# Optimization experiments

Hardware: AMD Instinct MI355X
Metric: run time of the kernel (lower is better)

The kernel has to match this reference:

```python
import jax, jax.numpy as jnp
import numpy as np
import math

B, S, D, H = 2, 1024, 4096, 32
HD = D // H          # head_dim = 128
P = 10               # prompt_len
THETA = 500000.0     # rope_theta


def _rope(t, cos, sin):
    # t: [b, s, h, hd]; pairs (2i, 2i+1) form complex numbers as in view_as_complex
    tr = t[..., 0::2]
    ti = t[..., 1::2]
    c = cos[None, :, None, :]
    s = sin[None, :, None, :]
    out = jnp.stack([tr * c - ti * s, tr * s + ti * c], axis=-1)  # [b,s,h,hd/2,2]
    return out.reshape(t.shape)


def setup_inputs() -> dict:
    key = jax.random.key(0)
    ks = jax.random.split(key, 8)
    sc = 0.02
    x = jax.random.normal(ks[0], (B, S, D), jnp.float32)
    wq = jax.random.normal(ks[1], (D, D), jnp.float32) * sc
    wk = jax.random.normal(ks[2], (D, D), jnp.float32) * sc
    wv = jax.random.normal(ks[3], (D, D), jnp.float32) * sc
    wo = jax.random.normal(ks[4], (D, D), jnp.float32) * sc
    prompt = jax.random.normal(ks[5], (P, D), jnp.float32)
    prompt_gate = jax.random.normal(ks[6], (1, H, 1, 1), jnp.float32) * 0.1
    # RoPE tables (real/imag of freqs_cis)
    inv = 1.0 / (THETA ** (jnp.arange(0, HD, 2, dtype=jnp.float32) / HD))  # [HD/2]
    ang = jnp.outer(jnp.arange(S, dtype=jnp.float32), inv)                 # [S, HD/2]
    freqs_cos = jnp.cos(ang)
    freqs_sin = jnp.sin(ang)
    # causal additive mask
    mask = jnp.triu(jnp.full((S, S), -1e9, jnp.float32), 1)[None, None]
    type_weight = jax.random.uniform(ks[7], (B, S, 1), jnp.float32)
    return dict(x=x, wq=wq, wk=wk, wv=wv, wo=wo, prompt=prompt,
                prompt_gate=prompt_gate, freqs_cos=freqs_cos,
                freqs_sin=freqs_sin, mask=mask, type_weight=type_weight,
                start_pos=0)


def reference(x, wq, wk, wv, wo, prompt, prompt_gate, freqs_cos, freqs_sin,
              mask, type_weight, start_pos):
    # training-mode forward: start_pos == 0, keys/values = current tokens
    scale = 1.0 / math.sqrt(HD)
    xq = (x @ wq.T).reshape(B, S, H, HD)
    xk = (x @ wk.T).reshape(B, S, H, HD)
    xv = (x @ wv.T).reshape(B, S, H, HD)
    xq = _rope(xq, freqs_cos, freqs_sin)
    xk = _rope(xk, freqs_cos, freqs_sin)
    q = xq.transpose(0, 2, 1, 3)  # [b,h,s,hd]
    k = xk.transpose(0, 2, 1, 3)
    v = xv.transpose(0, 2, 1, 3)
    scores = jnp.einsum('bhqd,bhkd->bhqk', q, k) * scale + mask
    probs = jax.nn.softmax(scores, axis=-1)
    out = jnp.einsum('bhqk,bhkd->bhqd', probs, v)  # [b,h,s,hd]
    # gated prompt injection (num_experts == 1); type_weight unused, as in source
    pk = (prompt @ wk.T).reshape(P, H, HD)
    pv = (prompt @ wv.T).reshape(P, H, HD)
    p_scores = jnp.einsum('bhqd,phd->bhqp', q, pk) * scale
    p_probs = prompt_gate * jax.nn.softmax(p_scores, axis=-1)
    p_out = jnp.einsum('bhqp,phd->bhqd', p_probs, pv)
    out = (out + p_out).transpose(0, 2, 1, 3).reshape(B, S, D)
    return out @ wo.T
```

## Files before the change

### kernel.cpp

```cpp
#include <hip/hip_runtime.h>
#include <hip/hip_bf16.h>
#include <stdint.h>

typedef __hip_bfloat16 bf16;
typedef __attribute__((ext_vector_type(8))) short short8;
typedef __attribute__((ext_vector_type(4))) float f32x4;

#define SCALE_ 0.08838834764831845f

static __device__ __forceinline__ float bf2f(short u) {
  unsigned int x = ((unsigned int)(unsigned short)u) << 16;
  return __builtin_bit_cast(float, x);
}
static __device__ __forceinline__ short f2bf(float f) {
  __hip_bfloat16 h = __float2bfloat16(f);
  return __builtin_bit_cast(short, h);
}
static __device__ __forceinline__ f32x4 mfma16(short8 a, short8 b, f32x4 c) {
  return __builtin_amdgcn_mfma_f32_16x16x32_bf16(a, b, c, 0, 0, 0);
}
static __device__ __forceinline__ void gl_lds16(const bf16* g, bf16* l) {
  __builtin_amdgcn_global_load_lds(
      (const __attribute__((address_space(1))) unsigned int*)g,
      (__attribute__((address_space(3))) unsigned int*)l, 16, 0, 0);
}

__global__ __launch_bounds__(256) void cvt6(
    const float* __restrict__ sx, const float* __restrict__ sq,
    const float* __restrict__ sk, const float* __restrict__ sv,
    const float* __restrict__ so, const float* __restrict__ sp,
    bf16* __restrict__ dx, bf16* __restrict__ dq, bf16* __restrict__ dk,
    bf16* __restrict__ dv, bf16* __restrict__ d4, bf16* __restrict__ dp)
{
  int b = blockIdx.x;
  const float* s; bf16* d; int off;
  if (b < 4096)       { s = sx; d = dx; off = b; }
  else if (b < 12288) { s = sq; d = dq; off = b - 4096; }
  else if (b < 20480) { s = sk; d = dk; off = b - 12288; }
  else if (b < 28672) { s = sv; d = dv; off = b - 20480; }
  else if (b < 36864) { s = so; d = d4; off = b - 28672; }
  else                { s = sp; d = dp; off = b - 36864; }
  long base = (long)off * 2048 + threadIdx.x * 8;
  f32x4 a = *(const f32x4*)(s + base);
  f32x4 c = *(const f32x4*)(s + base + 4);
  short8 o;
#pragma unroll
  for (int j = 0; j < 4; j++) { o[j] = f2bf(a[j]); o[4 + j] = f2bf(c[j]); }
  *(short8*)(d + base) = o;
}

template <int NKT, bool KSPLIT>
__global__ __launch_bounds__(512, 2) void gemm_bt(
    const bf16* __restrict__ A, const bf16* __restrict__ A2,
    const bf16* __restrict__ B0, const bf16* __restrict__ B1, const bf16* __restrict__ B2w,
    bf16* __restrict__ C0, bf16* __restrict__ C1, bf16* __restrict__ C2,
    bf16* __restrict__ P1, bf16* __restrict__ P2,
    float* __restrict__ CF,
    int M1, int Mtot)
{
  __shared__ char lds[131072];
  const int tid = threadIdx.x, w = tid >> 6, l = tid & 63;
  const int lr = l & 15, lg = l >> 4;
  const int wm = w >> 2, wn = w & 3;
  const int z = blockIdx.z;
  const bf16* Bw = KSPLIT ? B0 : ((z == 0) ? B0 : ((z == 1) ? B1 : B2w));
  bf16* C  = (z == 0) ? C0 : ((z == 1) ? C1 : C2);
  bf16* Cp = (KSPLIT || z == 0) ? (bf16*)0 : ((z == 1) ? P1 : P2);
  float* CFz = CF;
  long koff = 0;
  if (KSPLIT) { koff = (long)z * NKT * 64; CFz = CF + (long)z * M1 * 4096; }

  const int cpx = gridDim.x >> 3, orig = blockIdx.x;
  const int wg = (orig & 7) * cpx + (orig >> 3);
  const long m0 = (long)(wg >> 4) * 256;
  const long n0 = (long)(wg & 15) * 256;

  const int r0 = ((tid >> 3) << 1) | ((tid >> 2) & 1);
  const int c0 = (tid & 3) ^ ((tid >> 3) & 3);
  const bf16 *pa0, *pa1;
  {
    long mx = (long)(Mtot - M1) - 1;
    long g0 = m0 + r0, g1 = m0 + r0 + 128;
    const bf16 *q0, *q1;
    if (g0 < M1) q0 = A + g0 * 4096;
    else { long rr = g0 - M1; if (rr > mx) rr = mx; q0 = A2 + rr * 4096; }
    if (g1 < M1) q1 = A + g1 * 4096;
    else { long rr = g1 - M1; if (rr > mx) rr = mx; q1 = A2 + rr * 4096; }
    pa0 = q0 + c0 * 8 + koff;
    pa1 = q1 + c0 * 8 + koff;
  }
  const bf16* pb0 = Bw + (n0 + r0) * 4096 + c0 * 8 + koff;
  const bf16* pb1 = pb0 + (long)128 * 4096;

  const int ro  = (lr >> 1) * 128 + (((lr & 1) * 4) + (lg ^ ((lr >> 1) & 3))) * 16;
  const int aro = wm * 8192 + ro;
  const int bro = wn * 4096 + ro;

  f32x4 acc[8][4];
#pragma unroll
  for (int i = 0; i < 8; i++)
#pragma unroll
    for (int j = 0; j < 4; j++) acc[i][j] = (f32x4){0.f, 0.f, 0.f, 0.f};

  short8 af[4], bf[4];

#define STGA(S_, KE_)                                                        \
  {                                                                          \
    bf16* d_ = (bf16*)(lds + (S_) * 16384) + tid * 8;                        \
    gl_lds16(pa0 + (KE_), d_);                                               \
    gl_lds16(pa1 + (KE_), d_ + 4096);                                        \
  }
#define STGB(S_, KE_)                                                        \
  {                                                                          \
    bf16* d_ = (bf16*)(lds + (S_) * 16384) + tid * 8;                        \
    gl_lds16(pb0 + (KE_), d_);                                               \
    gl_lds16(pb1 + (KE_), d_ + 4096);                                        \
  }
#define SYNC(VM_)                                                            \
  {                                                                          \
    asm volatile("s_waitcnt vmcnt(" VM_ ")" ::: "memory");                   \
    __builtin_amdgcn_s_barrier();                                            \
    __builtin_amdgcn_sched_barrier(0);                                       \
  }
#define PHASE(PRB_, AU_, BU_, MO_, LB_, STG_)                                \
  {                                                                          \
    STG_                                                                     \
    const char* ab_ = lds + (PRB_) + (AU_) + aro;                            \
    _Pragma("unroll") for (int mi = 0; mi < 4; mi++)                         \
      af[mi] = *(const short8*)(ab_ + ((MO_) + mi) * 1024);                  \
    if (LB_) {                                                               \
      const char* bb_ = lds + (PRB_) + (BU_) + bro;                          \
      _Pragma("unroll") for (int ni = 0; ni < 4; ni++)                       \
        bf[ni] = *(const short8*)(bb_ + ni * 1024);                          \
    }                                                                        \
    asm volatile("s_waitcnt lgkmcnt(0)" ::: "memory");                       \
    __builtin_amdgcn_sched_barrier(0);                                       \
    __builtin_amdgcn_s_setprio(1);                                           \
    _Pragma("unroll") for (int mi = 0; mi < 4; mi++)                         \
      _Pragma("unroll") for (int ni = 0; ni < 4; ni++)                       \
        acc[(MO_) + mi][ni] = mfma16(af[mi], bf[ni], acc[(MO_) + mi][ni]);   \
    __builtin_amdgcn_s_setprio(0);                                           \
  }
#define KT(PRB_, S6_, S7_, S8_, S9_, KE1_, KE2_)                             \
  SYNC("8") PHASE(PRB_, 0, 16384, 0, 1, STGA(S6_, KE1_))                     \
  PHASE(PRB_, 0, 16384, 4, 0, STGB(S7_, KE1_))                               \
  SYNC("8") PHASE(PRB_, 32768, 49152, 0, 1, STGA(S8_, KE2_))                 \
  PHASE(PRB_, 32768, 49152, 4, 0, STGB(S9_, KE2_))

  STGA(0, 0) STGB(1, 0) STGA(2, 32) STGB(3, 32) STGA(4, 64) STGB(5, 64)

  for (int t = 0; t < NKT - 2; t += 2) {
    const int ka = (t + 1) * 64 + 32, kb = (t + 2) * 64;
    const int kc = (t + 2) * 64 + 32, kd = (t + 3) * 64;
    KT(0, 6, 7, 0, 1, ka, kb)
    KT(65536, 2, 3, 4, 5, kc, kd)
  }
  {
    const int kel = (NKT - 1) * 64 + 32;
    SYNC("8") PHASE(0, 0, 16384, 0, 1, STGA(6, kel))
    PHASE(0, 0, 16384, 4, 0, STGB(7, kel))
    SYNC("8") PHASE(0, 32768, 49152, 0, 1, )
    PHASE(0, 32768, 49152, 4, 0, )
  }
  SYNC("4") PHASE(65536, 0, 16384, 0, 1, )
  PHASE(65536, 0, 16384, 4, 0, )
  SYNC("0") PHASE(65536, 32768, 49152, 0, 1, )
  PHASE(65536, 32768, 49152, 4, 0, )

#undef KT
#undef PHASE
#undef SYNC
#undef STGB
#undef STGA

#pragma unroll
  for (int mi = 0; mi < 8; mi++) {
#pragma unroll
    for (int ni = 0; ni < 4; ni++) {
      long col = n0 + wn * 64 + ni * 16 + lr;
      f32x4 v = acc[mi][ni];
#pragma unroll
      for (int j = 0; j < 4; j++) {
        long row = m0 + wm * 128 + mi * 16 + lg * 4 + j;
        if (CFz) {
          CFz[row * 4096 + col] = v[j];
        } else if (row < M1) {
          *(short*)(C + row * 4096 + col) = f2bf(v[j]);
        } else if (Cp != 0 && row < Mtot) {
          *(short*)(Cp + (row - M1) * 4096 + col) = f2bf(v[j]);
        }
      }
    }
  }
}

__global__ __launch_bounds__(256) void addf(
    const float* __restrict__ p0, const float* __restrict__ p1,
    float* __restrict__ out)
{
  long i = ((long)blockIdx.x * 256 + threadIdx.x) * 4;
  f32x4 a = *(const f32x4*)(p0 + i);
  f32x4 b = *(const f32x4*)(p1 + i);
#pragma unroll
  for (int j = 0; j < 4; j++) a[j] += b[j];
  *(f32x4*)(out + i) = a;
}

__global__ __launch_bounds__(256) void rope_qk(
    bf16* __restrict__ Q, bf16* __restrict__ Kb,
    const float* __restrict__ FC, const float* __restrict__ FS)
{
  const int row = blockIdx.x;
  const int s = row & 1023;
  const int t = threadIdx.x;
  bf16* base = (blockIdx.y ? Kb : Q) + (long)row * 4096 + t * 16;
  short8 v0 = *(const short8*)base;
  short8 v1 = *(const short8*)(base + 8);
  const float* cp = FC + s * 64 + (t & 7) * 8;
  const float* sp = FS + s * 64 + (t & 7) * 8;
  f32x4 c0 = *(const f32x4*)cp;
  f32x4 c1 = *(const f32x4*)(cp + 4);
  f32x4 s0 = *(const f32x4*)sp;
  f32x4 s1 = *(const f32x4*)(sp + 4);
  short8 o0, o1;
#pragma unroll
  for (int j = 0; j < 4; j++) {
    float c = c0[j], sn = s0[j];
    float e = bf2f(v0[2 * j]), od = bf2f(v0[2 * j + 1]);
    o0[2 * j] = f2bf(e * c - od * sn);
    o0[2 * j + 1] = f2bf(e * sn + od * c);
    float c2 = c1[j], sn2 = s1[j];
    float e2 = bf2f(v1[2 * j]), od2 = bf2f(v1[2 * j + 1]);
    o1[2 * j] = f2bf(e2 * c2 - od2 * sn2);
    o1[2 * j + 1] = f2bf(e2 * sn2 + od2 * c2);
  }
  *(short8*)base = o0;
  *(short8*)(base + 8) = o1;
}

__global__ __launch_bounds__(256) void transpose_v(
    const bf16* __restrict__ V, bf16* __restrict__ VT)
{
  __shared__ bf16 T[64 * 128];
  const int tid = threadIdx.x;
  const int st = blockIdx.x * 64, bh = blockIdx.y;
  const int b = bh >> 5, h = bh & 31;
  const bf16* src = V + ((long)(b * 1024 + st)) * 4096 + h * 128;
#pragma unroll
  for (int rr = 0; rr < 4; ++rr) {
    int i = tid + rr * 256;
    int s_l = i >> 4, c = i & 15;
    short8 v = *(const short8*)(src + (long)s_l * 4096 + c * 8);
    *(short8*)((char*)T + s_l * 256 + ((c ^ (s_l & 7)) * 16)) = v;
  }
  __syncthreads();
#pragma unroll
  for (int rr = 0; rr < 4; ++rr) {
    int i = tid + rr * 256;
    int d = i >> 3, cs = i & 7;
    short8 ov;
#pragma unroll
    for (int e = 0; e < 8; e++) {
      int s_l = cs * 8 + e;
      ov[e] = *(const short*)((char*)T + s_l * 256 + (((d >> 3) ^ (s_l & 7)) * 16) + (d & 7) * 2);
    }
    *(short8*)(VT + ((long)bh * 128 + d) * 1024 + st + cs * 8) = ov;
  }
}

__global__ __launch_bounds__(256) void flash_attn(
    const bf16* __restrict__ Q, const bf16* __restrict__ Kg, const bf16* __restrict__ VT,
    const bf16* __restrict__ PK, const bf16* __restrict__ PV,
    const float* __restrict__ GATE, bf16* __restrict__ O)
{
  __shared__ bf16 Kl[32 * 128];
  __shared__ bf16 Vl[128 * 32];
  __shared__ bf16 PKl[16 * 128];
  __shared__ bf16 PVl[128 * 16];
  __shared__ bf16 Pl[4][16 * 32];
  const int tid = threadIdx.x, w = tid >> 6, l = tid & 63;
  const int lg = l >> 4, lr = l & 15;
  const int qb = blockIdx.x, bh = blockIdx.y;
  const int b = bh >> 5, h = bh & 31;
  const int q0 = qb * 64 + w * 16;

  short8 qf[4];
  {
    const bf16* qp = Q + ((long)(b * 1024 + q0 + lr)) * 4096 + h * 128 + lg * 8;
#pragma unroll
    for (int c = 0; c < 4; c++) qf[c] = *(const short8*)(qp + c * 32);
  }
  {
    int rowp = tid >> 4, pc = tid & 15, lc = pc ^ (rowp & 7);
    short8 v = {0, 0, 0, 0, 0, 0, 0, 0};
    if (rowp < 10) v = *(const short8*)(PK + (long)rowp * 4096 + h * 128 + lc * 8);
    *(short8*)((char*)PKl + tid * 16) = v;
  }
  {
    int d = tid >> 1, pb = (tid & 1) * 8;
#pragma unroll
    for (int e = 0; e < 8; e++) {
      int p = pb + e;
      short v = 0;
      if (p < 10) v = __builtin_bit_cast(short, PV[(long)p * 4096 + h * 128 + d]);
      *(short*)((char*)PVl + d * 32 + (((p >> 3) ^ (d & 1)) * 16) + (p & 7) * 2) = v;
    }
  }
  const float gate = GATE[h];

  f32x4 o[8];
#pragma unroll
  for (int i = 0; i < 8; i++) o[i] = (f32x4){0.f, 0.f, 0.f, 0.f};
  float m_[4] = {-1e30f, -1e30f, -1e30f, -1e30f};
  float l_[4] = {0.f, 0.f, 0.f, 0.f};

  const int nt = (qb + 1) * 2;
  const bf16* Kbase = Kg + ((long)b * 1024) * 4096 + h * 128;
  const bf16* Vbase = VT + ((long)bh) * 128 * 1024;
  const int cb1 = w * 64, cb2 = 256 + w * 64;
  const int iA = cb1 + l, iB = cb2 + l;
  bf16* pw = &Pl[w][0];

  for (int j = 0; j < nt; ++j) {
    __syncthreads();
    {
      const bf16* gA = Kbase + (long)(j * 32 + (iA >> 4)) * 4096 + ((iA & 15) ^ ((iA >> 4) & 7)) * 8;
      const bf16* gB = Kbase + (long)(j * 32 + (iB >> 4)) * 4096 + ((iB & 15) ^ ((iB >> 4) & 7)) * 8;
      gl_lds16(gA, Kl + cb1 * 8);
      gl_lds16(gB, Kl + cb2 * 8);
      const bf16* vA = Vbase + (long)(iA >> 2) * 1024 + j * 32 + ((iA & 3) ^ ((iA >> 2) & 3)) * 8;
      const bf16* vB = Vbase + (long)(iB >> 2) * 1024 + j * 32 + ((iB & 3) ^ ((iB >> 2) & 3)) * 8;
      gl_lds16(vA, Vl + cb1 * 8);
      gl_lds16(vB, Vl + cb2 * 8);
    }
    __syncthreads();

    f32x4 s[2];
#pragma unroll
    for (int ns = 0; ns < 2; ns++) {
      f32x4 a = (f32x4){0.f, 0.f, 0.f, 0.f};
      int krow = ns * 16 + lr;
      const char* kp = (const char*)Kl + krow * 256;
      int sw = krow & 7;
#pragma unroll
      for (int c = 0; c < 4; c++) {
        short8 kf = *(const short8*)(kp + (((c * 4 + lg) ^ sw) * 16));
        a = mfma16(qf[c], kf, a);
      }
      int key = j * 32 + krow;
#pragma unroll
      for (int r = 0; r < 4; r++) {
        int qr = q0 + lg * 4 + r;
        s[ns][r] = a[r] * SCALE_ + ((key <= qr) ? 0.0f : -1e30f);
      }
    }
    float mx[4], cor[4], sum[4];
#pragma unroll
    for (int r = 0; r < 4; r++) mx[r] = fmaxf(s[0][r], s[1][r]);
#pragma unroll
    for (int xm = 1; xm < 16; xm <<= 1)
#pragma unroll
      for (int r = 0; r < 4; r++) mx[r] = fmaxf(mx[r], __shfl_xor(mx[r], xm, 64));
#pragma unroll
    for (int r = 0; r < 4; r++) {
      float mn = fmaxf(m_[r], mx[r]);
      cor[r] = __expf(m_[r] - mn);
      m_[r] = mn;
      s[0][r] = __expf(s[0][r] - mn);
      s[1][r] = __expf(s[1][r] - mn);
      sum[r] = s[0][r] + s[1][r];
    }
#pragma unroll
    for (int xm = 1; xm < 16; xm <<= 1)
#pragma unroll
      for (int r = 0; r < 4; r++) sum[r] += __shfl_xor(sum[r], xm, 64);
#pragma unroll
    for (int r = 0; r < 4; r++) l_[r] = l_[r] * cor[r] + sum[r];
#pragma unroll
    for (int df = 0; df < 8; df++)
#pragma unroll
      for (int r = 0; r < 4; r++) o[df][r] *= cor[r];

#pragma unroll
    for (int ns = 0; ns < 2; ns++)
#pragma unroll
      for (int r = 0; r < 4; r++)
        *(short*)((char*)pw + ((lg * 4 + r) * 32 + ns * 16 + lr) * 2) = f2bf(s[ns][r]);
    asm volatile("s_waitcnt lgkmcnt(0)" ::: "memory");
    __builtin_amdgcn_sched_barrier(0);
    short8 pf = *(const short8*)(pw + lr * 32 + lg * 8);

#pragma unroll
    for (int df = 0; df < 8; df++) {
      int d = df * 16 + lr;
      short8 vf = *(const short8*)((const char*)Vl + d * 64 + ((lg ^ (d & 3)) * 16));
      o[df] = mfma16(pf, vf, o[df]);
    }
  }

  f32x4 ps;
  {
    f32x4 a = (f32x4){0.f, 0.f, 0.f, 0.f};
    const char* kp = (const char*)PKl + lr * 256;
    int sw = lr & 7;
#pragma unroll
    for (int c = 0; c < 4; c++) {
      short8 kf = *(const short8*)(kp + (((c * 4 + lg) ^ sw) * 16));
      a = mfma16(qf[c], kf, a);
    }
#pragma unroll
    for (int r = 0; r < 4; r++) ps[r] = (lr < 10) ? a[r] * SCALE_ : -1e30f;
  }
  {
    float pm[4], pss[4];
#pragma unroll
    for (int r = 0; r < 4; r++) pm[r] = ps[r];
#pragma unroll
    for (int xm = 1; xm < 16; xm <<= 1)
#pragma unroll
      for (int r = 0; r < 4; r++) pm[r] = fmaxf(pm[r], __shfl_xor(pm[r], xm, 64));
#pragma unroll
    for (int r = 0; r < 4; r++) { ps[r] = __expf(ps[r] - pm[r]); pss[r] = ps[r]; }
#pragma unroll
    for (int xm = 1; xm < 16; xm <<= 1)
#pragma unroll
      for (int r = 0; r < 4; r++) pss[r] += __shfl_xor(pss[r], xm, 64);
#pragma unroll
    for (int r = 0; r < 4; r++) ps[r] = ps[r] / pss[r];
  }
#pragma unroll
  for (int r = 0; r < 4; r++) {
    *(short*)((char*)pw + ((lg * 4 + r) * 32 + lr) * 2) = f2bf(ps[r]);
    *(short*)((char*)pw + ((lg * 4 + r) * 32 + 16 + lr) * 2) = 0;
  }
  asm volatile("s_waitcnt lgkmcnt(0)" ::: "memory");
  __builtin_amdgcn_sched_barrier(0);
  short8 pf2 = *(const short8*)(pw + lr * 32 + lg * 8);
  f32x4 po[8];
#pragma unroll
  for (int df = 0; df < 8; df++) {
    int d = df * 16 + lr;
    short8 vf = {0, 0, 0, 0, 0, 0, 0, 0};
    if (lg < 2) vf = *(const short8*)((const char*)PVl + d * 32 + ((lg ^ (d & 1)) * 16));
    po[df] = mfma16(pf2, vf, (f32x4){0.f, 0.f, 0.f, 0.f});
  }

  bf16* op = O + ((long)(b * 1024 + q0 + lg * 4)) * 4096 + h * 128 + lr;
#pragma unroll
  for (int df = 0; df < 8; df++)
#pragma unroll
    for (int r = 0; r < 4; r++) {
      float val = o[df][r] / l_[r] + gate * po[df][r];
      *(short*)(op + (long)r * 4096 + df * 16) = f2bf(val);
    }
}

extern "C" void kernel_launch(void* const* d_in, const int* in_sizes, int n_in,
                              void* d_out, int out_size, void* d_ws, size_t ws_size,
                              hipStream_t stream) {
  (void)in_sizes; (void)n_in; (void)out_size; (void)ws_size;
  const float* x      = (const float*)d_in[0];
  const float* wq     = (const float*)d_in[1];
  const float* wk     = (const float*)d_in[2];
  const float* wv     = (const float*)d_in[3];
  const float* wo     = (const float*)d_in[4];
  const float* prompt = (const float*)d_in[5];
  const float* gate   = (const float*)d_in[6];
  const float* fcos   = (const float*)d_in[7];
  const float* fsin   = (const float*)d_in[8];
  float* out = (float*)d_out;
  char* ws = (char*)d_ws;

  size_t o = 0;
  bf16* xb  = (bf16*)(ws + o); o += (size_t)8388608 * 2;
  bf16* wqb = (bf16*)(ws + o); o += (size_t)16777216 * 2;
  bf16* wkb = (bf16*)(ws + o); o += (size_t)16777216 * 2;
  bf16* wvb = (bf16*)(ws + o); o += (size_t)16777216 * 2;
  bf16* wob = (bf16*)(ws + o); o += (size_t)16777216 * 2;
  bf16* pb  = (bf16*)(ws + o); o += (size_t)40960 * 2;
  bf16* q_ws  = (bf16*)(ws + o); o += (size_t)2048 * 4096 * 2;
  bf16* k_ws  = (bf16*)(ws + o); o += (size_t)2048 * 4096 * 2;
  bf16* v_ws  = (bf16*)(ws + o); o += (size_t)2048 * 4096 * 2;
  bf16* vT_ws = (bf16*)(ws + o); o += (size_t)2048 * 4096 * 2;
  bf16* pk_ws = (bf16*)(ws + o); o += (size_t)40960 * 2;
  bf16* pv_ws = (bf16*)(ws + o); o += (size_t)40960 * 2;
  bf16* attn_ws = v_ws;
  float* p0 = (float*)q_ws;
  float* p1 = (float*)xb;

  cvt6<<<dim3(36884), 256, 0, stream>>>(x, wq, wk, wv, wo, prompt,
                                        xb, wqb, wkb, wvb, wob, pb);
  gemm_bt<64, false><<<dim3(144, 1, 3), 512, 0, stream>>>(
      xb, pb, wqb, wkb, wvb, q_ws, k_ws, v_ws, pk_ws, pv_ws, (float*)0, 2048, 2058);
  rope_qk<<<dim3(2048, 2), 256, 0, stream>>>(q_ws, k_ws, fcos, fsin);
  transpose_v<<<dim3(16, 64), 256, 0, stream>>>(v_ws, vT_ws);
  flash_attn<<<dim3(16, 64), 256, 0, stream>>>(
      q_ws, k_ws, vT_ws, pk_ws, pv_ws, gate, attn_ws);
  gemm_bt<32, true><<<dim3(128, 1, 2), 512, 0, stream>>>(
      attn_ws, attn_ws, wob, wob, wob, (bf16*)0, (bf16*)0, (bf16*)0,
      (bf16*)0, (bf16*)0, p0, 2048, 2048);
  addf<<<dim3(8192), 256, 0, stream>>>(p0, p0 + (size_t)2048 * 4096, out);
}
```

Before: 524.9 us.

## Replace split-K output GEMM with 256x128-tile kernel, fuse rope and V transpose

The output projection previously ran as a split-K GEMM writing two fp32 partials, followed by a separate add kernel. It now uses a dedicated 256x128-tile GEMM with a three-stage global-to-LDS pipeline and an XCD-aware block remap, writing fp32 output directly over the full K. This removes the partial-sum traffic and the extra launch, at the cost of fewer blocks (256) and a longer K loop per block. RoPE and the V transpose are also merged into one launch to save a kernel launch.

```diff
diff --git a/kernel.cpp b/kernel.cpp
--- a/kernel.cpp
+++ b/kernel.cpp
@@ -194,61 +194,154 @@
   }
 }
 
-__global__ __launch_bounds__(256) void addf(
-    const float* __restrict__ p0, const float* __restrict__ p1,
-    float* __restrict__ out)
+__global__ __launch_bounds__(512, 2) void gemm_n128(
+    const bf16* __restrict__ A, const bf16* __restrict__ Bw,
+    float* __restrict__ CF)
 {
-  long i = ((long)blockIdx.x * 256 + threadIdx.x) * 4;
-  f32x4 a = *(const f32x4*)(p0 + i);
-  f32x4 b = *(const f32x4*)(p1 + i);
-#pragma unroll
-  for (int j = 0; j < 4; j++) a[j] += b[j];
-  *(f32x4*)(out + i) = a;
-}
-
-__global__ __launch_bounds__(256) void rope_qk(
+  __shared__ char lds[98304];
+  const int tid = threadIdx.x, w = tid >> 6, l = tid & 63;
+  const int lr = l & 15, lg = l >> 4;
+  const int wm = w >> 1, wn = w & 1;
+
+  const int cpx = gridDim.x >> 3, orig = blockIdx.x;
+  const int wg = (orig & 7) * cpx + (orig >> 3);
+  const long m0 = (long)(wg >> 5) * 256;
+  const long n0 = (long)(wg & 31) * 128;
+
+  const int r0 = ((tid >> 3) << 1) | ((tid >> 2) & 1);
+  const int c0 = (tid & 3) ^ ((tid >> 3) & 3);
+  const bf16* pa0 = A + (m0 + r0) * 4096 + c0 * 8;
+  const bf16* pa1 = pa0 + (long)128 * 4096;
+  const bf16* pb0 = Bw + (n0 + r0) * 4096 + c0 * 8;
+
+  const int ro  = (lr >> 1) * 128 + (((lr & 1) * 4) + (lg ^ ((lr >> 1) & 3))) * 16;
+  const int aro = wm * 4096 + ro;
+  const int bro = wn * 4096 + ro;
+
+  f32x4 acc[4][4];
+#pragma unroll
+  for (int i = 0; i < 4; i++)
+#pragma unroll
+    for (int j = 0; j < 4; j++) acc[i][j] = (f32x4){0.f, 0.f, 0.f, 0.f};
+
+  short8 af[4], bf[4];
+
+#define NSTGA(SB_, KE_)                                                      \
+  {                                                                          \
+    bf16* d_ = (bf16*)(lds + (SB_)) + tid * 8;                               \
+    gl_lds16(pa0 + (KE_), d_);                                               \
+    gl_lds16(pa1 + (KE_), d_ + 4096);                                        \
+  }
+#define NSTGB(SB_, KE_)                                                      \
+  {                                                                          \
+    bf16* d_ = (bf16*)(lds + (SB_)) + tid * 8;                               \
+    gl_lds16(pb0 + (KE_), d_);                                               \
+  }
+#define NSYNC(VM_)                                                           \
+  {                                                                          \
+    asm volatile("s_waitcnt vmcnt(" VM_ ")" ::: "memory");                   \
+    __builtin_amdgcn_s_barrier();                                            \
+    __builtin_amdgcn_sched_barrier(0);                                       \
+  }
+#define NPH(PRB_, AO_, BO_, STG_)                                            \
+  {                                                                          \
+    STG_                                                                     \
+    const char* ab_ = lds + (PRB_) + (AO_) + aro;                            \
+    _Pragma("unroll") for (int mi = 0; mi < 4; mi++)                         \
+      af[mi] = *(const short8*)(ab_ + mi * 1024);                            \
+    const char* bb_ = lds + (PRB_) + (BO_) + bro;                            \
+    _Pragma("unroll") for (int ni = 0; ni < 4; ni++)                         \
+      bf[ni] = *(const short8*)(bb_ + ni * 1024);                            \
+    asm volatile("s_waitcnt lgkmcnt(0)" ::: "memory");                       \
+    __builtin_amdgcn_sched_barrier(0);                                       \
+    __builtin_amdgcn_s_setprio(1);                                           \
+    _Pragma("unroll") for (int mi = 0; mi < 4; mi++)                         \
+      _Pragma("unroll") for (int ni = 0; ni < 4; ni++)                       \
+        acc[mi][ni] = mfma16(af[mi], bf[ni], acc[mi][ni]);                   \
+    __builtin_amdgcn_s_setprio(0);                                           \
+  }
+
+  NSTGA(0, 0)      NSTGB(16384, 0)
+  NSTGA(24576, 32) NSTGB(40960, 32)
+  NSTGA(49152, 64) NSTGB(65536, 64)
+
+  for (int t = 0; t < 62; t += 2) {
+    const int ka = (t + 1) * 64 + 32;
+    const int kb = (t + 2) * 64;
+    NSYNC("3") NPH(0, 0, 16384,     NSTGA(49152 + 24576, ka) NSTGB(49152 + 40960, ka))
+    NSYNC("3") NPH(0, 24576, 40960, NSTGA(0, kb) NSTGB(16384, kb))
+    const int kc = (t + 2) * 64 + 32;
+    const int kd = (t + 3) * 64;
+    NSYNC("3") NPH(49152, 0, 16384,     NSTGA(24576, kc) NSTGB(40960, kc))
+    NSYNC("3") NPH(49152, 24576, 40960, NSTGA(49152, kd) NSTGB(49152 + 16384, kd))
+  }
+  NSYNC("3") NPH(0, 0, 16384,     NSTGA(49152 + 24576, 63 * 64 + 32) NSTGB(49152 + 40960, 63 * 64 + 32))
+  NSYNC("3") NPH(0, 24576, 40960, )
+  NSYNC("3") NPH(49152, 0, 16384, )
+  NSYNC("0") NPH(49152, 24576, 40960, )
+
+#undef NPH
+#undef NSYNC
+#undef NSTGB
+#undef NSTGA
+
+#pragma unroll
+  for (int mi = 0; mi < 4; mi++) {
+#pragma unroll
+    for (int ni = 0; ni < 4; ni++) {
+      long col = n0 + wn * 64 + ni * 16 + lr;
+      f32x4 v = acc[mi][ni];
+#pragma unroll
+      for (int j = 0; j < 4; j++) {
+        long row = m0 + wm * 64 + mi * 16 + lg * 4 + j;
+        CF[row * 4096 + col] = v[j];
+      }
+    }
+  }
+}
+
+__global__ __launch_bounds__(256) void prep_qkv(
     bf16* __restrict__ Q, bf16* __restrict__ Kb,
-    const float* __restrict__ FC, const float* __restrict__ FS)
-{
-  const int row = blockIdx.x;
-  const int s = row & 1023;
-  const int t = threadIdx.x;
-  bf16* base = (blockIdx.y ? Kb : Q) + (long)row * 4096 + t * 16;
-  short8 v0 = *(const short8*)base;
-  short8 v1 = *(const short8*)(base + 8);
-  const float* cp = FC + s * 64 + (t & 7) * 8;
-  const float* sp = FS + s * 64 + (t & 7) * 8;
-  f32x4 c0 = *(const f32x4*)cp;
-  f32x4 c1 = *(const f32x4*)(cp + 4);
-  f32x4 s0 = *(const f32x4*)sp;
-  f32x4 s1 = *(const f32x4*)(sp + 4);
-  short8 o0, o1;
-#pragma unroll
-  for (int j = 0; j < 4; j++) {
-    float c = c0[j], sn = s0[j];
-    float e = bf2f(v0[2 * j]), od = bf2f(v0[2 * j + 1]);
-    o0[2 * j] = f2bf(e * c - od * sn);
-    o0[2 * j + 1] = f2bf(e * sn + od * c);
-    float c2 = c1[j], sn2 = s1[j];
-    float e2 = bf2f(v1[2 * j]), od2 = bf2f(v1[2 * j + 1]);
-    o1[2 * j] = f2bf(e2 * c2 - od2 * sn2);
-    o1[2 * j + 1] = f2bf(e2 * sn2 + od2 * c2);
-  }
-  *(short8*)base = o0;
-  *(short8*)(base + 8) = o1;
-}
-
-__global__ __launch_bounds__(256) void transpose_v(
+    const float* __restrict__ FC, const float* __restrict__ FS,
     const bf16* __restrict__ V, bf16* __restrict__ VT)
 {
+  const int t = threadIdx.x;
+  if (blockIdx.y < 2) {
+    const int row = blockIdx.x;
+    const int s = row & 1023;
+    bf16* base = (blockIdx.y ? Kb : Q) + (long)row * 4096 + t * 16;
+    short8 v0 = *(const short8*)base;
+    short8 v1 = *(const short8*)(base + 8);
+    const float* cp = FC + s * 64 + (t & 7) * 8;
+    const float* sp = FS + s * 64 + (t & 7) * 8;
+    f32x4 c0 = *(const f32x4*)cp;
+    f32x4 c1 = *(const f32x4*)(cp + 4);
+    f32x4 s0 = *(const f32x4*)sp;
+    f32x4 s1 = *(const f32x4*)(sp + 4);
+    short8 o0, o1;
+#pragma unroll
+    for (int j = 0; j < 4; j++) {
+      float c = c0[j], sn = s0[j];
+      float e = bf2f(v0[2 * j]), od = bf2f(v0[2 * j + 1]);
+      o0[2 * j] = f2bf(e * c - od * sn);
+      o0[2 * j + 1] = f2bf(e * sn + od * c);
+      float c2 = c1[j], sn2 = s1[j];
+      float e2 = bf2f(v1[2 * j]), od2 = bf2f(v1[2 * j + 1]);
+      o1[2 * j] = f2bf(e2 * c2 - od2 * sn2);
+      o1[2 * j + 1] = f2bf(e2 * sn2 + od2 * c2);
+    }
+    *(short8*)base = o0;
+    *(short8*)(base + 8) = o1;
+    return;
+  }
+  if (blockIdx.x >= 1024) return;
   __shared__ bf16 T[64 * 128];
-  const int tid = threadIdx.x;
-  const int st = blockIdx.x * 64, bh = blockIdx.y;
+  const int st = (blockIdx.x & 15) * 64, bh = blockIdx.x >> 4;
   const int b = bh >> 5, h = bh & 31;
   const bf16* src = V + ((long)(b * 1024 + st)) * 4096 + h * 128;
 #pragma unroll
   for (int rr = 0; rr < 4; ++rr) {
-    int i = tid + rr * 256;
+    int i = t + rr * 256;
     int s_l = i >> 4, c = i & 15;
     short8 v = *(const short8*)(src + (long)s_l * 4096 + c * 8);
     *(short8*)((char*)T + s_l * 256 + ((c ^ (s_l & 7)) * 16)) = v;
@@ -256,7 +349,7 @@
   __syncthreads();
 #pragma unroll
   for (int rr = 0; rr < 4; ++rr) {
-    int i = tid + rr * 256;
+    int i = t + rr * 256;
     int d = i >> 3, cs = i & 7;
     short8 ov;
 #pragma unroll
@@ -485,19 +578,13 @@
   bf16* pk_ws = (bf16*)(ws + o); o += (size_t)40960 * 2;
   bf16* pv_ws = (bf16*)(ws + o); o += (size_t)40960 * 2;
   bf16* attn_ws = v_ws;
-  float* p0 = (float*)q_ws;
-  float* p1 = (float*)xb;
 
   cvt6<<<dim3(36884), 256, 0, stream>>>(x, wq, wk, wv, wo, prompt,
                                         xb, wqb, wkb, wvb, wob, pb);
   gemm_bt<64, false><<<dim3(144, 1, 3), 512, 0, stream>>>(
       xb, pb, wqb, wkb, wvb, q_ws, k_ws, v_ws, pk_ws, pv_ws, (float*)0, 2048, 2058);
-  rope_qk<<<dim3(2048, 2), 256, 0, stream>>>(q_ws, k_ws, fcos, fsin);
-  transpose_v<<<dim3(16, 64), 256, 0, stream>>>(v_ws, vT_ws);
+  prep_qkv<<<dim3(2048, 3), 256, 0, stream>>>(q_ws, k_ws, fcos, fsin, v_ws, vT_ws);
   flash_attn<<<dim3(16, 64), 256, 0, stream>>>(
       q_ws, k_ws, vT_ws, pk_ws, pv_ws, gate, attn_ws);
-  gemm_bt<32, true><<<dim3(128, 1, 2), 512, 0, stream>>>(
-      attn_ws, attn_ws, wob, wob, wob, (bf16*)0, (bf16*)0, (bf16*)0,
-      (bf16*)0, (bf16*)0, p0, 2048, 2048);
-  addf<<<dim3(8192), 256, 0, stream>>>(p0, p0 + (size_t)2048 * 4096, out);
-}
+  gemm_n128<<<dim3(256), 512, 0, stream>>>(attn_ws, wob, out);
+}
```

New measurement: 508.3 us. -3.2%, faster.
